# Kernel optimization log

Measured on AMD Instinct MI355X. Metric: run time of the kernel, lower is better.

Reference implementation:

```python
import jax, jax.numpy as jnp
import numpy as np
import math

B, N, D_MODEL = 1, 2925, 1536
NUM_HEADS, HEAD_DIM = 12, 128
F, H, W = 13, 15, 15
MAX_SEQ = 1024
EPS = 1e-6


def _make_freqs(max_seq, dim):
    # (cos, sin) pairs for half-dim rotary frequencies, base 10000
    inv = 1.0 / (10000.0 ** (np.arange(0, dim, 2, dtype=np.float64) / dim))
    ang = np.arange(max_seq, dtype=np.float64)[:, None] * inv[None, :]
    return jnp.asarray(np.stack([np.cos(ang), np.sin(ang)], axis=-1), dtype=jnp.float32)


def setup_inputs() -> dict:
    key = jax.random.key(0)
    ks = jax.random.split(key, 10)
    s = 1.0 / math.sqrt(D_MODEL)
    dim_base = HEAD_DIM // 6              # 21
    dim_t = HEAD_DIM - 4 * dim_base       # 44
    dim_h = 2 * dim_base                  # 42
    return {
        "x": jax.random.normal(ks[0], (B, N, D_MODEL), dtype=jnp.float32),
        "Wq": jax.random.normal(ks[1], (D_MODEL, D_MODEL), dtype=jnp.float32) * s,
        "bq": jnp.zeros((D_MODEL,), dtype=jnp.float32),
        "Wk": jax.random.normal(ks[2], (D_MODEL, D_MODEL), dtype=jnp.float32) * s,
        "bk": jnp.zeros((D_MODEL,), dtype=jnp.float32),
        "Wv": jax.random.normal(ks[3], (D_MODEL, D_MODEL), dtype=jnp.float32) * s,
        "bv": jnp.zeros((D_MODEL,), dtype=jnp.float32),
        "Wo": jax.random.normal(ks[4], (D_MODEL, D_MODEL), dtype=jnp.float32) * s,
        "bo": jnp.zeros((D_MODEL,), dtype=jnp.float32),
        "q_scale": jnp.ones((D_MODEL,), dtype=jnp.float32),
        "k_scale": jnp.ones((D_MODEL,), dtype=jnp.float32),
        "freqs_t": _make_freqs(MAX_SEQ, dim_t),
        "freqs_h": _make_freqs(MAX_SEQ, dim_h),
        "freqs_w": _make_freqs(MAX_SEQ, dim_h),
        "f": F, "h": H, "w": W,
    }


def _rms_norm(x, scale, eps=EPS):
    var = jnp.mean(jnp.square(x), axis=-1, keepdims=True)
    return x * jax.lax.rsqrt(var + eps) * scale


def _rope_apply(x, f, h, w, freqs_t, freqs_h, freqs_w):
    # x: [b, n, H, D] with n == f*h*w
    b, n, nh, d = x.shape
    db = d // 6
    dt, dh, dw = d - 4 * db, 2 * db, 2 * db
    ft = jnp.broadcast_to(freqs_t[:f, None, None, :, :], (f, h, w, dt // 2, 2))
    fh = jnp.broadcast_to(freqs_h[None, :h, None, :, :], (f, h, w, dh // 2, 2))
    fw = jnp.broadcast_to(freqs_w[None, None, :w, :, :], (f, h, w, dw // 2, 2))
    fg = jnp.concatenate([ft, fh, fw], axis=3).reshape(n, d // 2, 2)[None, :, None, :, :]
    xc = x.reshape(b, n, nh, d // 2, 2)
    re = xc[..., 0] * fg[..., 0] - xc[..., 1] * fg[..., 1]
    im = xc[..., 0] * fg[..., 1] + xc[..., 1] * fg[..., 0]
    return jnp.stack([re, im], axis=-1).reshape(b, n, nh, d)


def reference(x, Wq, bq, Wk, bk, Wv, bv, Wo, bo, q_scale, k_scale,
              freqs_t, freqs_h, freqs_w, f, h, w):
    b, n, _ = x.shape
    nh, d = NUM_HEADS, HEAD_DIM
    # projections + RMSNorm across full hidden dim (before head split)
    q = _rms_norm(x @ Wq + bq, q_scale).reshape(b, n, nh, d)
    k = _rms_norm(x @ Wk + bk, k_scale).reshape(b, n, nh, d)
    v = (x @ Wv + bv).reshape(b, n, nh, d)
    # 3D RoPE on [b, n, H, D] layout
    q = _rope_apply(q, f, h, w, freqs_t, freqs_h, freqs_w)
    k = _rope_apply(k, f, h, w, freqs_t, freqs_h, freqs_w)
    # [b, H, n, d]
    q = q.transpose(0, 2, 1, 3)
    k = k.transpose(0, 2, 1, 3)
    v = v.transpose(0, 2, 1, 3)
    scores = jnp.einsum("bhid,bhjd->bhij", q, k) / math.sqrt(d)
    attn = jax.nn.softmax(scores, axis=-1)
    out = jnp.einsum("bhij,bhjd->bhid", attn, v)
    out = out.transpose(0, 2, 1, 3).reshape(b, n, nh * d)
    return out @ Wo + bo
```

## Files before the change

### kernel.cpp

```cpp
#include <hip/hip_runtime.h>


#define N_TOK 2925
#define DMODEL 1536
#define NHEAD 12
#define HDIM 128
#define KSPLIT 1472
#define VT_STRIDE 2944

typedef __attribute__((ext_vector_type(8))) __bf16 bf16x8;
typedef __attribute__((ext_vector_type(4))) float floatx4;

#define MFMA(a, b, c) __builtin_amdgcn_mfma_f32_16x16x32_bf16((a), (b), (c), 0, 0, 0)

static __device__ __forceinline__ unsigned short f2bf(float f) {
    unsigned u = __builtin_bit_cast(unsigned, f);
    return (unsigned short)((u + 0x7fffu + ((u >> 16) & 1u)) >> 16);
}

static __device__ __forceinline__ void gload_lds16(const unsigned short* g, unsigned short* l) {
    __builtin_amdgcn_global_load_lds((const __attribute__((address_space(1))) void*)g,
                                     (__attribute__((address_space(3))) void*)l, 16, 0, 0);
}

__global__ __launch_bounds__(256) void k_convert_x(const float* __restrict__ x,
                                                   unsigned short* __restrict__ xb, int n) {
    int i = (blockIdx.x * 256 + threadIdx.x) * 4;
    if (i < n) {
        float4 v = *(const float4*)(x + i);
        uint2 o;
        o.x = (unsigned)f2bf(v.x) | ((unsigned)f2bf(v.y) << 16);
        o.y = (unsigned)f2bf(v.z) | ((unsigned)f2bf(v.w) << 16);
        *(uint2*)(xb + i) = o;
    }
}

__global__ __launch_bounds__(256) void k_transpose_w(const float* __restrict__ W0,
                                                     const float* __restrict__ W1,
                                                     const float* __restrict__ W2,
                                                     const float* __restrict__ W3,
                                                     unsigned short* __restrict__ Wt) {
    __shared__ float tile[32][33];
    const float* W = blockIdx.z == 0 ? W0 : blockIdx.z == 1 ? W1 : blockIdx.z == 2 ? W2 : W3;
    unsigned short* out = Wt + (size_t)blockIdx.z * DMODEL * DMODEL;
    int tx = threadIdx.x, ty = threadIdx.y;
    int bx = blockIdx.x * 32, by = blockIdx.y * 32;
#pragma unroll
    for (int i = 0; i < 4; i++)
        tile[ty + 8 * i][tx] = W[(size_t)(by + ty + 8 * i) * DMODEL + bx + tx];
    __syncthreads();
#pragma unroll
    for (int i = 0; i < 4; i++)
        out[(size_t)(bx + ty + 8 * i) * DMODEL + by + tx] = f2bf(tile[tx][ty + 8 * i]);
}

__global__ __launch_bounds__(256, 3) void k_gemm(const unsigned short* __restrict__ A,
                                                 const unsigned short* __restrict__ BtBase,
                                                 const float* __restrict__ b0,
                                                 const float* __restrict__ b1,
                                                 const float* __restrict__ b2,
                                                 float* __restrict__ Cbase, int M) {
    const int nbx = gridDim.x, nxy = gridDim.x * gridDim.y;
    const int nb = nxy * gridDim.z;
    {
    }
    const int blin = blockIdx.x + nbx * (blockIdx.y + gridDim.y * blockIdx.z);
    const int q8 = nb >> 3, r8 = nb & 7, xcd = blin & 7, idx = blin >> 3;
    const int wg = (xcd < r8) ? xcd * (q8 + 1) + idx
                              : r8 * (q8 + 1) + (xcd - r8) * q8 + idx;
    const int z = wg / nxy;
    const int rem = wg % nxy;
    const int bym = rem / nbx, bxn = rem % nbx;

    const unsigned short* Bt = BtBase + (size_t)z * DMODEL * DMODEL;
    const float* bias = (z == 0) ? b0 : (z == 1) ? b1 : b2;
    float* C = Cbase + (size_t)z * M * DMODEL;

    __shared__ __align__(16) unsigned short As[128 * 32];
    __shared__ __align__(16) unsigned short Bs[128 * 32];

    const int tid = threadIdx.x;
    const int wave = tid >> 6, lane = tid & 63, quad = lane >> 4, l16 = lane & 15;
    const int wr = wave >> 1, wc = wave & 1;
    const int m0 = bym * 128, n0 = bxn * 128;

    const int r4 = tid >> 2, c4 = (tid & 3) * 8;

    floatx4 acc[4][4] = {};

    for (int k0 = 0; k0 < DMODEL; k0 += 32) {
        gload_lds16(A + (size_t)(m0 + r4) * DMODEL + k0 + c4,       &As[r4 * 32 + c4]);
        gload_lds16(A + (size_t)(m0 + r4 + 64) * DMODEL + k0 + c4,  &As[(r4 + 64) * 32 + c4]);
        gload_lds16(Bt + (size_t)(n0 + r4) * DMODEL + k0 + c4,      &Bs[r4 * 32 + c4]);
        gload_lds16(Bt + (size_t)(n0 + r4 + 64) * DMODEL + k0 + c4, &Bs[(r4 + 64) * 32 + c4]);
        __syncthreads();

        bf16x8 af[4], bfm[4];
#pragma unroll
        for (int i = 0; i < 4; i++)
            af[i] = *(const bf16x8*)&As[(wr * 64 + i * 16 + l16) * 32 + quad * 8];
#pragma unroll
        for (int j = 0; j < 4; j++)
            bfm[j] = *(const bf16x8*)&Bs[(wc * 64 + j * 16 + l16) * 32 + quad * 8];
#pragma unroll
        for (int i = 0; i < 4; i++)
#pragma unroll
            for (int j = 0; j < 4; j++)
                acc[i][j] = MFMA(af[i], bfm[j], acc[i][j]);
        __syncthreads();
    }

#pragma unroll
    for (int j = 0; j < 4; j++) {
        int cg = n0 + wc * 64 + j * 16 + l16;
        float bv = bias[cg];
#pragma unroll
        for (int i = 0; i < 4; i++) {
            int rbase = m0 + wr * 64 + i * 16 + quad * 4;
#pragma unroll
            for (int r = 0; r < 4; r++) {
                int rg = rbase + r;
                if (rg < M) C[(size_t)rg * DMODEL + cg] = acc[i][j][r] + bv;
            }
        }
    }
}

__global__ __launch_bounds__(256) void k_norm_rope(const float* __restrict__ Qf,
                                                   const float* __restrict__ Kf,
                                                   const float* __restrict__ Vf,
                                                   const float* __restrict__ qsc,
                                                   const float* __restrict__ ksc,
                                                   const float* __restrict__ ft,
                                                   const float* __restrict__ fh,
                                                   const float* __restrict__ fw,
                                                   unsigned short* __restrict__ qb,
                                                   unsigned short* __restrict__ kb,
                                                   unsigned short* __restrict__ vb) {
    const int n = blockIdx.x;
    const int tid = threadIdx.x, wave = tid >> 6, lane = tid & 63;
    const int t_i = n / 225, rem = n % 225, h_i = rem / 15, w_i = rem % 15;
    const float att_scale = 0.08838834764831845f * 1.4426950408889634f;

    float2 qv[3], kv[3], vv[3];
    float sq = 0.f, sk = 0.f;
#pragma unroll
    for (int c = 0; c < 3; c++) {
        int p = tid + 256 * c;
        qv[c] = *(const float2*)(Qf + (size_t)n * DMODEL + 2 * p);
        kv[c] = *(const float2*)(Kf + (size_t)n * DMODEL + 2 * p);
        vv[c] = *(const float2*)(Vf + (size_t)n * DMODEL + 2 * p);
        sq += qv[c].x * qv[c].x + qv[c].y * qv[c].y;
        sk += kv[c].x * kv[c].x + kv[c].y * kv[c].y;
    }
#pragma unroll
    for (int off = 32; off >= 1; off >>= 1) {
        sq += __shfl_xor(sq, off, 64);
        sk += __shfl_xor(sk, off, 64);
    }
    __shared__ float red[2][4];
    if (lane == 0) { red[0][wave] = sq; red[1][wave] = sk; }
    __syncthreads();
    sq = red[0][0] + red[0][1] + red[0][2] + red[0][3];
    sk = red[1][0] + red[1][1] + red[1][2] + red[1][3];
    const float rq = rsqrtf(sq * (1.f / 1536.f) + 1e-6f) * att_scale;
    const float rk = rsqrtf(sk * (1.f / 1536.f) + 1e-6f);

#pragma unroll
    for (int c = 0; c < 3; c++) {
        int p = tid + 256 * c;
        int hd = p >> 6, pl = p & 63, dd = 2 * pl;
        float cs, sn;
        if (pl < 22)      { cs = ft[t_i * 44 + 2 * pl];        sn = ft[t_i * 44 + 2 * pl + 1]; }
        else if (pl < 43) { int pp = pl - 22; cs = fh[h_i * 42 + 2 * pp]; sn = fh[h_i * 42 + 2 * pp + 1]; }
        else              { int pp = pl - 43; cs = fw[w_i * 42 + 2 * pp]; sn = fw[w_i * 42 + 2 * pp + 1]; }
        int hidx = hd * 128 + dd;
        float q0 = qv[c].x * rq * qsc[hidx], q1 = qv[c].y * rq * qsc[hidx + 1];
        float k0 = kv[c].x * rk * ksc[hidx], k1 = kv[c].y * rk * ksc[hidx + 1];
        size_t o = ((size_t)hd * N_TOK + n) * HDIM + dd;
        unsigned qo = (unsigned)f2bf(q0 * cs - q1 * sn) | ((unsigned)f2bf(q0 * sn + q1 * cs) << 16);
        unsigned ko = (unsigned)f2bf(k0 * cs - k1 * sn) | ((unsigned)f2bf(k0 * sn + k1 * cs) << 16);
        unsigned vo = (unsigned)f2bf(vv[c].x) | ((unsigned)f2bf(vv[c].y) << 16);
        *(unsigned*)(qb + o) = qo;
        *(unsigned*)(kb + o) = ko;
        *(unsigned*)(vb + o) = vo;
    }
}

__global__ __launch_bounds__(256) void k_transpose_v(const unsigned short* __restrict__ vbi,
                                                     unsigned short* __restrict__ vt) {
    __shared__ unsigned short tile[32][33];
    const int head = blockIdx.z;
    const int t0 = blockIdx.x * 32, d0 = blockIdx.y * 32;
    const int tx = threadIdx.x, ty = threadIdx.y;
#pragma unroll
    for (int i = 0; i < 4; i++) {
        int t = t0 + ty + 8 * i;
        tile[ty + 8 * i][tx] = (t < N_TOK) ? vbi[((size_t)head * N_TOK + t) * HDIM + d0 + tx] : 0;
    }
    __syncthreads();
    int t = t0 + tx;
#pragma unroll
    for (int i = 0; i < 4; i++)
        vt[((size_t)head * HDIM + d0 + ty + 8 * i) * VT_STRIDE + t] = tile[tx][ty + 8 * i];
}

__global__ __launch_bounds__(256, 4) void k_attn_part(const unsigned short* __restrict__ qb,
                                                      const unsigned short* __restrict__ kb,
                                                      const unsigned short* __restrict__ vt,
                                                      float* __restrict__ Opart,
                                                      float* __restrict__ mbuf,
                                                      float* __restrict__ lbuf) {
    __shared__ __align__(16) unsigned short Ks[64 * 128];
    __shared__ __align__(16) unsigned short Vs[128 * 64];
    __shared__ __align__(16) unsigned short Ps[4][16 * 64];

    const int b = blockIdx.x + 46 * (blockIdx.y + 12 * (int)blockIdx.z);
    const int w = (b & 7) * 138 + (b >> 3);
    const int qblk = w % 46;
    const int head = (w / 46) % 12;
    const int z    = w / 552;

    const int tid = threadIdx.x, wave = tid >> 6, lane = tid & 63;
    const int quad = lane >> 4, l16 = lane & 15, x7 = l16 & 7;
    const int q0 = qblk * 64 + wave * 16;
    const unsigned short* qh = qb + (size_t)head * N_TOK * HDIM;
    const unsigned short* kh = kb + (size_t)head * N_TOK * HDIM;
    const unsigned short* vh = vt + (size_t)head * HDIM * VT_STRIDE;
    unsigned short* ps = Ps[wave];

    const int kbeg = z ? KSPLIT : 0;
    const int kend = z ? N_TOK : KSPLIT;
    const int ntile = (kend - kbeg + 63) >> 6;

    int koff[4];
#pragma unroll
    for (int ks = 0; ks < 4; ks++) {
        int c = ks * 4 + quad;
        koff[ks] = ((c & 8) | ((c & 7) ^ x7)) * 8;
    }
    const int pwq = (quad >> 1), pwh = (quad & 1) * 4;

    const int krow = tid >> 4, ksw = tid & 15;
    const int kc = (ksw & 8) | ((ksw & 7) ^ (krow & 7));
    const int vd = tid >> 3, vsw = tid & 7;
    const int vc = vsw ^ (vd & 7);
    const unsigned short* ksrc = kh + (size_t)krow * HDIM + kc * 8;
    const unsigned short* vsrc = vh + (size_t)vd * VT_STRIDE + vc * 8;

    bf16x8 aq[4];
    {
        int qrow = q0 + l16;
        if (qrow < N_TOK) {
#pragma unroll
            for (int ks = 0; ks < 4; ks++)
                aq[ks] = *(const bf16x8*)&qh[(size_t)qrow * HDIM + ks * 32 + quad * 8];
        } else {
#pragma unroll
            for (int ks = 0; ks < 4; ks++) aq[ks] = (bf16x8)(__bf16)0.0f;
        }
    }

    floatx4 oacc[8] = {};
    float m_l = -1e30f;
    float l_l = 0.f;

    {
        const bool part0 = (kbeg + 64 > kend);
        if (!part0) {
#pragma unroll
            for (int i = 0; i < 4; i++)
                gload_lds16(ksrc + (size_t)(kbeg + 16 * i) * HDIM, &Ks[(tid + 256 * i) * 8]);
        } else {
#pragma unroll
            for (int i = 0; i < 4; i++) {
                int gk = kbeg + krow + 16 * i;
                gk = gk < N_TOK ? gk : N_TOK - 1;
                gload_lds16(kh + (size_t)gk * HDIM + kc * 8, &Ks[(tid + 256 * i) * 8]);
            }
        }
#pragma unroll
        for (int i = 0; i < 4; i++)
            gload_lds16(vsrc + (size_t)(32 * i) * VT_STRIDE + kbeg, &Vs[(tid + 256 * i) * 8]);
    }

    for (int t = 0; t < ntile; t++) {
        const int kb0 = kbeg + t * 64;
        const bool fullt = (kb0 + 64 <= kend);
        const bool has_next = (t + 1 < ntile);

        asm volatile("s_waitcnt vmcnt(4)" ::: "memory");
        __builtin_amdgcn_sched_barrier(0);
        __builtin_amdgcn_s_barrier();

        floatx4 sa[4] = {};
        __builtin_amdgcn_s_setprio(1);
#pragma unroll
        for (int j = 0; j < 4; j++)
#pragma unroll
            for (int ks = 0; ks < 4; ks++) {
                bf16x8 bkf = *(const bf16x8*)&Ks[(j * 16 + l16) * HDIM + koff[ks]];
                sa[j] = MFMA(bkf, aq[ks], sa[j]);
            }
        __builtin_amdgcn_s_setprio(0);
        __builtin_amdgcn_s_barrier();

        if (has_next) {
            const int kn = kb0 + 64;
            if (kn + 64 <= kend) {
#pragma unroll
                for (int i = 0; i < 4; i++)
                    gload_lds16(ksrc + (size_t)(kn + 16 * i) * HDIM, &Ks[(tid + 256 * i) * 8]);
            } else {
#pragma unroll
                for (int i = 0; i < 4; i++) {
                    int gk = kn + krow + 16 * i;
                    gk = gk < N_TOK ? gk : N_TOK - 1;
                    gload_lds16(kh + (size_t)gk * HDIM + kc * 8, &Ks[(tid + 256 * i) * 8]);
                }
            }
        }

        float mt;
        if (fullt) {
            float m01 = fmaxf(fmaxf(sa[0][0], sa[0][1]), fmaxf(sa[0][2], sa[0][3]));
            float m23 = fmaxf(fmaxf(sa[1][0], sa[1][1]), fmaxf(sa[1][2], sa[1][3]));
            float m45 = fmaxf(fmaxf(sa[2][0], sa[2][1]), fmaxf(sa[2][2], sa[2][3]));
            float m67 = fmaxf(fmaxf(sa[3][0], sa[3][1]), fmaxf(sa[3][2], sa[3][3]));
            mt = fmaxf(fmaxf(m01, m23), fmaxf(m45, m67));
        } else {
            mt = -1e30f;
            const int kq = kb0 + quad * 4;
#pragma unroll
            for (int j = 0; j < 4; j++)
#pragma unroll
                for (int r = 0; r < 4; r++)
                    mt = fmaxf(mt, (kq + j * 16 + r < kend) ? sa[j][r] : -1e30f);
        }
        mt = fmaxf(mt, __shfl_xor(mt, 16));
        mt = fmaxf(mt, __shfl_xor(mt, 32));

        if (__any(mt > m_l + 8.f)) {
            float mn = fmaxf(m_l, mt);
            float alpha = exp2f(m_l - mn);
            m_l = mn;
            l_l *= alpha;
#pragma unroll
            for (int r = 0; r < 4; r++) {
                float ar = __shfl(alpha, quad * 4 + r, 16);
#pragma unroll
                for (int jd = 0; jd < 8; jd++) oacc[jd][r] *= ar;
            }
        }

        if (fullt) {
#pragma unroll
            for (int j = 0; j < 4; j++) {
                float p0 = exp2f(sa[j][0] - m_l), p1 = exp2f(sa[j][1] - m_l);
                float p2 = exp2f(sa[j][2] - m_l), p3 = exp2f(sa[j][3] - m_l);
                l_l += (p0 + p1) + (p2 + p3);
                uint2 wv;
                wv.x = (unsigned)__builtin_bit_cast(unsigned short, (__bf16)p0) |
                       ((unsigned)__builtin_bit_cast(unsigned short, (__bf16)p1) << 16);
                wv.y = (unsigned)__builtin_bit_cast(unsigned short, (__bf16)p2) |
                       ((unsigned)__builtin_bit_cast(unsigned short, (__bf16)p3) << 16);
                *(uint2*)&ps[l16 * 64 + (((j * 2 + pwq) ^ x7) << 3) + pwh] = wv;
            }
        } else {
            const int kq = kb0 + quad * 4;
#pragma unroll
            for (int j = 0; j < 4; j++) {
                float p[4];
#pragma unroll
                for (int r = 0; r < 4; r++) {
                    p[r] = (kq + j * 16 + r < kend) ? exp2f(sa[j][r] - m_l) : 0.f;
                    l_l += p[r];
                }
                uint2 wv;
                wv.x = (unsigned)__builtin_bit_cast(unsigned short, (__bf16)p[0]) |
                       ((unsigned)__builtin_bit_cast(unsigned short, (__bf16)p[1]) << 16);
                wv.y = (unsigned)__builtin_bit_cast(unsigned short, (__bf16)p[2]) |
                       ((unsigned)__builtin_bit_cast(unsigned short, (__bf16)p[3]) << 16);
                *(uint2*)&ps[l16 * 64 + (((j * 2 + pwq) ^ x7) << 3) + pwh] = wv;
            }
        }

        if (has_next) { asm volatile("s_waitcnt vmcnt(4)" ::: "memory"); }
        else          { asm volatile("s_waitcnt vmcnt(0)" ::: "memory"); }
        __builtin_amdgcn_sched_barrier(0);
        __builtin_amdgcn_s_barrier();

        __builtin_amdgcn_s_setprio(1);
#pragma unroll
        for (int ks = 0; ks < 2; ks++) {
            bf16x8 ap = *(const bf16x8*)&ps[l16 * 64 + koff[ks]];
#pragma unroll
            for (int jd = 0; jd < 8; jd++) {
                bf16x8 bvf = *(const bf16x8*)&Vs[(jd * 16 + l16) * 64 + koff[ks]];
                oacc[jd] = MFMA(ap, bvf, oacc[jd]);
            }
        }
        __builtin_amdgcn_s_setprio(0);
        __builtin_amdgcn_s_barrier();

        if (has_next) {
            const int kn = kb0 + 64;
#pragma unroll
            for (int i = 0; i < 4; i++)
                gload_lds16(vsrc + (size_t)(32 * i) * VT_STRIDE + kn, &Vs[(tid + 256 * i) * 8]);
        }
    }

    l_l += __shfl_xor(l_l, 16);
    l_l += __shfl_xor(l_l, 32);

#pragma unroll
    for (int r = 0; r < 4; r++) {
        int rg = q0 + quad * 4 + r;
        if (rg < N_TOK) {
            size_t rbase = ((size_t)(z * NHEAD + head) * N_TOK + rg) * HDIM;
#pragma unroll
            for (int jd = 0; jd < 8; jd++)
                Opart[rbase + jd * 16 + l16] = oacc[jd][r];
        }
    }
    if (quad == 0 && q0 + l16 < N_TOK) {
        int mi = (z * NHEAD + head) * N_TOK + q0 + l16;
        mbuf[mi] = m_l;
        lbuf[mi] = l_l;
    }
}

__global__ __launch_bounds__(256) void k_combine(const float* __restrict__ Opart,
                                                 const float* __restrict__ mbuf,
                                                 const float* __restrict__ lbuf,
                                                 unsigned short* __restrict__ ab) {
    const int R = NHEAD * N_TOK;
    int r = blockIdx.x * 8 + (threadIdx.x >> 5);
    if (r >= R) return;
    int l32 = threadIdx.x & 31;
    float m0 = mbuf[r], m1 = mbuf[R + r];
    float l0 = lbuf[r], l1 = lbuf[R + r];
    float m = fmaxf(m0, m1);
    float w0 = exp2f(m0 - m), w1 = exp2f(m1 - m);
    float inv = 1.f / (l0 * w0 + l1 * w1);
    w0 *= inv; w1 *= inv;
    float4 a = *(const float4*)&Opart[(size_t)r * HDIM + l32 * 4];
    float4 b = *(const float4*)&Opart[((size_t)R + r) * HDIM + l32 * 4];
    int head = r / N_TOK, tok = r % N_TOK;
    unsigned short* o = ab + (size_t)tok * DMODEL + head * HDIM + l32 * 4;
    uint2 pk;
    pk.x = (unsigned)f2bf(a.x * w0 + b.x * w1) | ((unsigned)f2bf(a.y * w0 + b.y * w1) << 16);
    pk.y = (unsigned)f2bf(a.z * w0 + b.z * w1) | ((unsigned)f2bf(a.w * w0 + b.w * w1) << 16);
    *(uint2*)o = pk;
}

extern "C" void kernel_launch(void* const* d_in, const int* in_sizes, int n_in,
                              void* d_out, int out_size, void* d_ws, size_t ws_size,
                              hipStream_t stream) {
    const float* x   = (const float*)d_in[0];
    const float* Wq  = (const float*)d_in[1];
    const float* bq  = (const float*)d_in[2];
    const float* Wk  = (const float*)d_in[3];
    const float* bk  = (const float*)d_in[4];
    const float* Wv  = (const float*)d_in[5];
    const float* bv  = (const float*)d_in[6];
    const float* Wo  = (const float*)d_in[7];
    const float* bo  = (const float*)d_in[8];
    const float* qsc = (const float*)d_in[9];
    const float* ksc = (const float*)d_in[10];
    const float* ft  = (const float*)d_in[11];
    const float* fh  = (const float*)d_in[12];
    const float* fw  = (const float*)d_in[13];

    char* ws = (char*)d_ws;
    unsigned short* xb   = (unsigned short*)ws; ws += (size_t)N_TOK * DMODEL * 2;
    unsigned short* Wt   = (unsigned short*)ws; ws += (size_t)4 * DMODEL * DMODEL * 2;
    unsigned short* ab   = (unsigned short*)ws; ws += (size_t)N_TOK * DMODEL * 2;
    char* qkvf_region    = ws;                  ws += (size_t)3 * N_TOK * DMODEL * 4;
    unsigned short* qkvb = (unsigned short*)ws; ws += (size_t)3 * N_TOK * DMODEL * 2;

    float* Qf = (float*)qkvf_region;
    float* Kf = Qf + (size_t)N_TOK * DMODEL;
    float* Vf = Qf + (size_t)2 * N_TOK * DMODEL;
    float* Opart = (float*)qkvf_region;
    float* mbuf  = Opart + (size_t)2 * NHEAD * N_TOK * HDIM;
    float* lbuf  = mbuf + (size_t)2 * NHEAD * N_TOK;
    unsigned short* vtp = (unsigned short*)(lbuf + (size_t)2 * NHEAD * N_TOK);

    unsigned short* qbp = qkvb;
    unsigned short* kbp = qkvb + (size_t)N_TOK * DMODEL;
    unsigned short* vbp = qkvb + (size_t)2 * N_TOK * DMODEL;

    const int nelem = N_TOK * DMODEL;
    k_convert_x<<<(nelem / 4 + 255) / 256, 256, 0, stream>>>(x, xb, nelem);
    k_transpose_w<<<dim3(48, 48, 4), dim3(32, 8), 0, stream>>>(Wq, Wk, Wv, Wo, Wt);
    k_gemm<<<dim3(12, 23, 3), 256, 0, stream>>>(xb, Wt, bq, bk, bv, Qf, N_TOK);
    k_norm_rope<<<N_TOK, 256, 0, stream>>>(Qf, Kf, Vf, qsc, ksc, ft, fh, fw, qbp, kbp, vbp);
    k_transpose_v<<<dim3(92, 4, NHEAD), dim3(32, 8), 0, stream>>>(vbp, vtp);
    k_attn_part<<<dim3(46, NHEAD, 2), 256, 0, stream>>>(qbp, kbp, vtp, Opart, mbuf, lbuf);
    k_combine<<<(NHEAD * N_TOK + 7) / 8, 256, 0, stream>>>(Opart, mbuf, lbuf, ab);
    k_gemm<<<dim3(12, 23, 1), 256, 0, stream>>>(ab, Wt + (size_t)3 * DMODEL * DMODEL,
                                                bo, bo, bo, (float*)d_out, N_TOK);
}
```

Measured before the change: 368.0 us.

## Add 256x256-tile double-buffered QKV GEMM kernel with swizzled LDS

Replaces the 128x128-tile QKV projection GEMM with a dedicated 512-thread kernel. Each block computes a 256x256 output tile. K steps of 64 are double-buffered in LDS with XOR-swizzled layout, and global-to-LDS loads are interleaved with MFMA phases using barriers and s_setprio. The larger tile is meant to raise data reuse and overlap memory with compute. In exchange it launches only 216 blocks, which under-fills the CUs. The tail M tile also reads A rows beyond the token count; those results are discarded by the guarded stores.

After: 355.6 us. 3.4% less time.

```diff
diff --git a/kernel.cpp b/kernel.cpp
--- a/kernel.cpp
+++ b/kernel.cpp
@@ -54,6 +54,156 @@
         out[(size_t)(bx + ty + 8 * i) * DMODEL + by + tx] = f2bf(tile[tx][ty + 8 * i]);
 }
 
+__global__ __launch_bounds__(512, 2) void k_gemm_qkv(const unsigned short* __restrict__ A,
+                                                     const unsigned short* __restrict__ BtBase,
+                                                     const float* __restrict__ b0,
+                                                     const float* __restrict__ b1,
+                                                     const float* __restrict__ b2,
+                                                     float* __restrict__ Cbase, int M) {
+    __shared__ __align__(16) unsigned short As[2][256 * 64];
+    __shared__ __align__(16) unsigned short Bs[2][256 * 64];
+
+    const int blin = blockIdx.x + 6 * (blockIdx.y + 12 * (int)blockIdx.z);
+    const int wg = (blin & 7) * 27 + (blin >> 3);
+    const int z = wg / 72, rem = wg % 72, mt = rem / 6, ntile = rem % 6;
+    const unsigned short* Bt = BtBase + (size_t)z * DMODEL * DMODEL;
+    const float* bias = (z == 0) ? b0 : (z == 1) ? b1 : b2;
+    float* C = Cbase + (size_t)z * M * DMODEL;
+    const int m0 = mt * 256, n0 = ntile * 256;
+
+    const int tid = threadIdx.x;
+    const int wave = tid >> 6, lane = tid & 63, quad = lane >> 4, l16 = lane & 15;
+    const int x7 = l16 & 7;
+    const int wm = wave >> 2, wn = wave & 3;
+
+    const int koff0 = ((quad) ^ x7) * 8;
+    const int koff1 = ((4 + quad) ^ x7) * 8;
+
+    const int sl = tid & 7;
+
+    floatx4 acc[8][4] = {};
+
+    const unsigned short* Abase = A + (size_t)m0 * DMODEL;
+    const unsigned short* Bbase = Bt + (size_t)n0 * DMODEL;
+
+    auto stageB = [&](int buf, int h, int kt) {
+#pragma unroll
+        for (int i = 0; i < 2; i++) {
+            int d = tid + 512 * i;
+            int row = h * 128 + (d >> 3);
+            int c = sl ^ (row & 7);
+            gload_lds16(Bbase + (size_t)row * DMODEL + kt * 64 + c * 8,
+                        &Bs[buf][(row * 8 + sl) * 8]);
+        }
+    };
+    auto stageA = [&](int buf, int h, int kt) {
+#pragma unroll
+        for (int i = 0; i < 2; i++) {
+            int d = tid + 512 * i;
+            int r7 = d >> 3;
+            int row = (r7 & 63) + h * 64 + (r7 >> 6) * 128;
+            int c = sl ^ (row & 7);
+            gload_lds16(Abase + (size_t)row * DMODEL + kt * 64 + c * 8,
+                        &As[buf][(row * 8 + sl) * 8]);
+        }
+    };
+
+    stageB(0, 0, 0); stageB(0, 1, 0); stageA(0, 0, 0); stageA(0, 1, 0);
+
+    const int NT = DMODEL / 64;
+    for (int t = 0; t < NT; t++) {
+        const int c = t & 1, sb = c ^ 1;
+        const int ts = (t + 1 < NT) ? t + 1 : NT - 1;
+
+        asm volatile("s_waitcnt vmcnt(2)" ::: "memory");
+        __builtin_amdgcn_sched_barrier(0);
+        __builtin_amdgcn_s_barrier();
+
+        bf16x8 af[4], bfm[4];
+#pragma unroll
+        for (int m = 0; m < 4; m++)
+            af[m] = *(const bf16x8*)&As[c][(wm * 128 + m * 16 + l16) * 64 + koff0];
+#pragma unroll
+        for (int n = 0; n < 4; n++)
+            bfm[n] = *(const bf16x8*)&Bs[c][(wn * 64 + n * 16 + l16) * 64 + koff0];
+        stageB(sb, 0, ts);
+        __builtin_amdgcn_s_barrier();
+        __builtin_amdgcn_s_setprio(1);
+#pragma unroll
+        for (int m = 0; m < 4; m++)
+#pragma unroll
+            for (int n = 0; n < 4; n++)
+                acc[m][n] = MFMA(af[m], bfm[n], acc[m][n]);
+        __builtin_amdgcn_s_setprio(0);
+        __builtin_amdgcn_sched_barrier(0);
+
+        asm volatile("s_waitcnt vmcnt(2)" ::: "memory");
+        __builtin_amdgcn_sched_barrier(0);
+        __builtin_amdgcn_s_barrier();
+
+        bf16x8 af2[4];
+#pragma unroll
+        for (int m = 0; m < 4; m++)
+            af2[m] = *(const bf16x8*)&As[c][(wm * 128 + 64 + m * 16 + l16) * 64 + koff0];
+        stageB(sb, 1, ts);
+        __builtin_amdgcn_s_barrier();
+        __builtin_amdgcn_s_setprio(1);
+#pragma unroll
+        for (int m = 0; m < 4; m++)
+#pragma unroll
+            for (int n = 0; n < 4; n++)
+                acc[4 + m][n] = MFMA(af2[m], bfm[n], acc[4 + m][n]);
+        __builtin_amdgcn_s_setprio(0);
+        __builtin_amdgcn_sched_barrier(0);
+
+#pragma unroll
+        for (int m = 0; m < 4; m++)
+            af[m] = *(const bf16x8*)&As[c][(wm * 128 + m * 16 + l16) * 64 + koff1];
+#pragma unroll
+        for (int n = 0; n < 4; n++)
+            bfm[n] = *(const bf16x8*)&Bs[c][(wn * 64 + n * 16 + l16) * 64 + koff1];
+        stageA(sb, 0, ts);
+        __builtin_amdgcn_s_barrier();
+        __builtin_amdgcn_s_setprio(1);
+#pragma unroll
+        for (int m = 0; m < 4; m++)
+#pragma unroll
+            for (int n = 0; n < 4; n++)
+                acc[m][n] = MFMA(af[m], bfm[n], acc[m][n]);
+        __builtin_amdgcn_s_setprio(0);
+        __builtin_amdgcn_sched_barrier(0);
+
+#pragma unroll
+        for (int m = 0; m < 4; m++)
+            af2[m] = *(const bf16x8*)&As[c][(wm * 128 + 64 + m * 16 + l16) * 64 + koff1];
+        stageA(sb, 1, ts);
+        __builtin_amdgcn_s_barrier();
+        __builtin_amdgcn_s_setprio(1);
+#pragma unroll
+        for (int m = 0; m < 4; m++)
+#pragma unroll
+            for (int n = 0; n < 4; n++)
+                acc[4 + m][n] = MFMA(af2[m], bfm[n], acc[4 + m][n]);
+        __builtin_amdgcn_s_setprio(0);
+        __builtin_amdgcn_sched_barrier(0);
+    }
+
+#pragma unroll
+    for (int n = 0; n < 4; n++) {
+        int cg = n0 + wn * 64 + n * 16 + l16;
+        float bv = bias[cg];
+#pragma unroll
+        for (int m = 0; m < 8; m++) {
+            int rbase = m0 + wm * 128 + m * 16 + quad * 4;
+#pragma unroll
+            for (int r = 0; r < 4; r++) {
+                int rg = rbase + r;
+                if (rg < M) C[(size_t)rg * DMODEL + cg] = acc[m][n][r] + bv;
+            }
+        }
+    }
+}
+
 __global__ __launch_bounds__(256, 3) void k_gemm(const unsigned short* __restrict__ A,
                                                  const unsigned short* __restrict__ BtBase,
                                                  const float* __restrict__ b0,
@@ -62,8 +212,6 @@
                                                  float* __restrict__ Cbase, int M) {
     const int nbx = gridDim.x, nxy = gridDim.x * gridDim.y;
     const int nb = nxy * gridDim.z;
-    {
-    }
     const int blin = blockIdx.x + nbx * (blockIdx.y + gridDim.y * blockIdx.z);
     const int q8 = nb >> 3, r8 = nb & 7, xcd = blin & 7, idx = blin >> 3;
     const int wg = (xcd < r8) ? xcd * (q8 + 1) + idx
@@ -83,7 +231,6 @@
     const int wave = tid >> 6, lane = tid & 63, quad = lane >> 4, l16 = lane & 15;
     const int wr = wave >> 1, wc = wave & 1;
     const int m0 = bym * 128, n0 = bxn * 128;
-
     const int r4 = tid >> 2, c4 = (tid & 3) * 8;
 
     floatx4 acc[4][4] = {};
@@ -495,7 +642,7 @@
     const int nelem = N_TOK * DMODEL;
     k_convert_x<<<(nelem / 4 + 255) / 256, 256, 0, stream>>>(x, xb, nelem);
     k_transpose_w<<<dim3(48, 48, 4), dim3(32, 8), 0, stream>>>(Wq, Wk, Wv, Wo, Wt);
-    k_gemm<<<dim3(12, 23, 3), 256, 0, stream>>>(xb, Wt, bq, bk, bv, Qf, N_TOK);
+    k_gemm_qkv<<<dim3(6, 12, 3), 512, 0, stream>>>(xb, Wt, bq, bk, bv, Qf, N_TOK);
     k_norm_rope<<<N_TOK, 256, 0, stream>>>(Qf, Kf, Vf, qsc, ksc, ft, fh, fw, qbp, kbp, vbp);
     k_transpose_v<<<dim3(92, 4, NHEAD), dim3(32, 8), 0, stream>>>(vbp, vtp);
     k_attn_part<<<dim3(46, NHEAD, 2), 256, 0, stream>>>(qbp, kbp, vtp, Opart, mbuf, lbuf);
```
